# Performance work log

Hardware: AMD Instinct MI355X
Metric: run time of the kernel (lower is better)

## Reference

```python
import jax, jax.numpy as jnp
import numpy as np

# Module constants (from init_kwargs)
P = 0.1          # deletion probability (error_prob)
B, L, V = 4096, 128, 64   # batch, max_len, vocab_size


def setup_inputs() -> dict:
    key = jax.random.key(0)
    k1, k2, k3 = jax.random.split(key, 3)
    # messages/probs are relaxed one-hot distributions over the vocab
    messages = jax.nn.softmax(jax.random.normal(k1, (B, L, V), dtype=jnp.float32), axis=-1)
    probs = jax.nn.softmax(jax.random.normal(k2, (B, L, V), dtype=jnp.float32), axis=-1)
    # Bernoulli(P) deletion targets (module draws these from its own generator)
    target_mask = jax.random.uniform(k3, (B, L)) < P
    return {"messages": messages, "probs": probs, "target_mask": target_mask}


def _process_noise(messages, probs, target_mask):
    """Training-mode DeletionChannel.gs with apply_noise=True.

    The torch shift() loop (O(L) sequential masked rolls) is exactly stream
    compaction: kept symbols move to the front in order, and the last
    n_deleted positions are overwritten with the EOS one-hot [1,0,...,0].
    A single stable argsort on the deletion mask gives destination order.
    """
    _, Ln, Vn = messages.shape
    # stable sort keys: kept (0) before deleted (1), order preserved within each
    order = jnp.argsort(target_mask.astype(jnp.int32), axis=1, stable=True)  # [B,L]
    shifted = jnp.take_along_axis(messages, order[:, :, None], axis=1)        # [B,L,V]
    n_deleted = target_mask.sum(axis=1, keepdims=True)                        # [B,1]
    # positions j with (L-1-j) < n_deleted  <=>  j >= L - n_deleted
    eos_tail = jnp.arange(Ln)[None, :] >= (Ln - n_deleted)                    # [B,L]
    eos = jnp.zeros((Vn,), messages.dtype).at[0].set(1.0)
    out_messages = jnp.where(eos_tail[:, :, None], eos, shifted)
    # probs: non-EOS mass scaled by (1-p); EOS absorbs the remainder
    tail = probs[..., 1:] * (1.0 - P)
    out_probs = jnp.concatenate([1.0 - tail.sum(-1, keepdims=True), tail], axis=-1)
    return out_messages, out_probs


def reference(messages, probs, target_mask):
    # forward() returns (process(noise=True), process(noise=False));
    # the noise-free branch is the identity, so we return the noisy pair
    # stacked into one array: [2, B, L, V].
    out_m, out_p = _process_noise(messages, probs, target_mask)
    return jnp.stack([out_m, out_p])
```

## Files before the change

### kernel.cpp

```cpp
#include <hip/hip_runtime.h>

constexpr int Bn = 4096;
constexpr int Ln = 128;
constexpr int Vn = 64;
constexpr float KEEP = 0.9f;

__global__ __launch_bounds__(256) void deletion_channel_kernel(
    const float* __restrict__ msgs,
    const float* __restrict__ probs,
    const int* __restrict__ mask,
    float* __restrict__ out)
{
    const int b   = blockIdx.x;
    const int tid = threadIdx.x;
    const int lane = tid & 63;
    const int wave = tid >> 6;

    __shared__ int s_src[Ln];
    __shared__ int s_wavecnt[2];

    bool kept = false;
    int rank = 0;
    if (tid < Ln) kept = (mask[(size_t)b * Ln + tid] == 0);
    if (wave < 2) {
        unsigned long long bal = __ballot(kept);
        rank = __popcll(bal & ((1ull << lane) - 1ull));
        if (lane == 0) s_wavecnt[wave] = (int)__popcll(bal);
    }
    __syncthreads();
    if (tid < Ln && kept) {
        const int off = (wave == 1) ? s_wavecnt[0] : 0;
        s_src[off + rank] = tid;
    }
    __syncthreads();
    const int nkept = s_wavecnt[0] + s_wavecnt[1];

    const size_t rowbase = (size_t)b * (Ln * Vn);

    {
        const float4* __restrict__ src4 = (const float4*)(msgs + rowbase);
        float4* __restrict__ dst4       = (float4*)(out + rowbase);
        constexpr int TOT4 = Ln * Vn / 4;
        #pragma unroll
        for (int it = 0; it < TOT4 / 256; ++it) {
            const int idx = it * 256 + tid;
            const int j = idx >> 4;
            const int q = idx & 15;
            float4 v;
            if (j < nkept) {
                v = src4[(s_src[j] << 4) + q];
            } else {
                v = make_float4((q == 0) ? 1.0f : 0.0f, 0.0f, 0.0f, 0.0f);
            }
            dst4[idx] = v;
        }
    }

    {
        const float4* __restrict__ src4 = (const float4*)(probs + rowbase);
        float4* __restrict__ dst4 = (float4*)(out + (size_t)Bn * Ln * Vn + rowbase);
        constexpr int TOT4 = Ln * Vn / 4;
        #pragma unroll
        for (int it = 0; it < TOT4 / 256; ++it) {
            const int idx = it * 256 + tid;
            const int q = idx & 15;
            const float4 p = src4[idx];
            float s = p.x + p.y + p.z + p.w;
            if (q == 0) s -= p.x;
            s += __shfl_xor(s, 1);
            s += __shfl_xor(s, 2);
            s += __shfl_xor(s, 4);
            s += __shfl_xor(s, 8);
            float4 o = make_float4(p.x * KEEP, p.y * KEEP, p.z * KEEP, p.w * KEEP);
            if (q == 0) o.x = 1.0f - KEEP * s;
            dst4[idx] = o;
        }
    }
}

extern "C" void kernel_launch(void* const* d_in, const int* in_sizes, int n_in,
                              void* d_out, int out_size, void* d_ws, size_t ws_size,
                              hipStream_t stream) {
    const float* msgs  = (const float*)d_in[0];
    const float* probs = (const float*)d_in[1];
    const int*   mask  = (const int*)d_in[2];
    float* out = (float*)d_out;

    deletion_channel_kernel<<<Bn, 256, 0, stream>>>(msgs, probs, mask, out);
}
```

Before: 430.4 us.

## Split into separate msgs/probs kernels with nontemporal loads and stores

Splits the fused kernel into two launches: one compacts messages per batch row, the other processes probs over two rows per block. All global loads and stores become nontemporal builtins on ext_vector float4 types, so the streaming data bypasses cache retention. The probs kernel no longer waits on the mask prefix or the shared-memory syncs. In exchange it adds a second kernel launch and drops the overlap of the two streams within one block.

```diff
diff --git a/kernel.cpp b/kernel.cpp
--- a/kernel.cpp
+++ b/kernel.cpp
@@ -5,14 +5,15 @@
 constexpr int Vn = 64;
 constexpr float KEEP = 0.9f;
 
-__global__ __launch_bounds__(256) void deletion_channel_kernel(
+typedef float f32x4 __attribute__((ext_vector_type(4)));
+
+__global__ __launch_bounds__(256) void deletion_msgs_kernel(
     const float* __restrict__ msgs,
-    const float* __restrict__ probs,
     const int* __restrict__ mask,
     float* __restrict__ out)
 {
-    const int b   = blockIdx.x;
-    const int tid = threadIdx.x;
+    const int b    = blockIdx.x;
+    const int tid  = threadIdx.x;
     const int lane = tid & 63;
     const int wave = tid >> 6;
 
@@ -36,45 +37,47 @@
     const int nkept = s_wavecnt[0] + s_wavecnt[1];
 
     const size_t rowbase = (size_t)b * (Ln * Vn);
+    const f32x4* __restrict__ src4 = (const f32x4*)(msgs + rowbase);
+    f32x4* __restrict__ dst4       = (f32x4*)(out + rowbase);
+    constexpr int TOT4 = Ln * Vn / 4;
+    #pragma unroll
+    for (int it = 0; it < TOT4 / 256; ++it) {
+        const int idx = it * 256 + tid;
+        const int j = idx >> 4;
+        const int q = idx & 15;
+        f32x4 v;
+        if (j < nkept) {
+            v = __builtin_nontemporal_load(&src4[(s_src[j] << 4) + q]);
+        } else {
+            v = (f32x4){(q == 0) ? 1.0f : 0.0f, 0.0f, 0.0f, 0.0f};
+        }
+        __builtin_nontemporal_store(v, &dst4[idx]);
+    }
+}
 
-    {
-        const float4* __restrict__ src4 = (const float4*)(msgs + rowbase);
-        float4* __restrict__ dst4       = (float4*)(out + rowbase);
-        constexpr int TOT4 = Ln * Vn / 4;
-        #pragma unroll
-        for (int it = 0; it < TOT4 / 256; ++it) {
-            const int idx = it * 256 + tid;
-            const int j = idx >> 4;
-            const int q = idx & 15;
-            float4 v;
-            if (j < nkept) {
-                v = src4[(s_src[j] << 4) + q];
-            } else {
-                v = make_float4((q == 0) ? 1.0f : 0.0f, 0.0f, 0.0f, 0.0f);
-            }
-            dst4[idx] = v;
-        }
-    }
-
-    {
-        const float4* __restrict__ src4 = (const float4*)(probs + rowbase);
-        float4* __restrict__ dst4 = (float4*)(out + (size_t)Bn * Ln * Vn + rowbase);
-        constexpr int TOT4 = Ln * Vn / 4;
-        #pragma unroll
-        for (int it = 0; it < TOT4 / 256; ++it) {
-            const int idx = it * 256 + tid;
-            const int q = idx & 15;
-            const float4 p = src4[idx];
-            float s = p.x + p.y + p.z + p.w;
-            if (q == 0) s -= p.x;
-            s += __shfl_xor(s, 1);
-            s += __shfl_xor(s, 2);
-            s += __shfl_xor(s, 4);
-            s += __shfl_xor(s, 8);
-            float4 o = make_float4(p.x * KEEP, p.y * KEEP, p.z * KEEP, p.w * KEEP);
-            if (q == 0) o.x = 1.0f - KEEP * s;
-            dst4[idx] = o;
-        }
+__global__ __launch_bounds__(256) void deletion_probs_kernel(
+    const float* __restrict__ probs,
+    float* __restrict__ out)
+{
+    const int tid = threadIdx.x;
+    const size_t base = (size_t)blockIdx.x * (2 * Ln * Vn / 4);
+    const f32x4* __restrict__ src4 = (const f32x4*)probs + base;
+    f32x4* __restrict__ dst4 = (f32x4*)(out + (size_t)Bn * Ln * Vn) + base;
+    constexpr int TOT4 = 2 * Ln * Vn / 4;
+    #pragma unroll
+    for (int it = 0; it < TOT4 / 256; ++it) {
+        const int idx = it * 256 + tid;
+        const int q = idx & 15;
+        const f32x4 p = __builtin_nontemporal_load(&src4[idx]);
+        float s = p.x + p.y + p.z + p.w;
+        if (q == 0) s -= p.x;
+        s += __shfl_xor(s, 1);
+        s += __shfl_xor(s, 2);
+        s += __shfl_xor(s, 4);
+        s += __shfl_xor(s, 8);
+        f32x4 o = p * KEEP;
+        if (q == 0) o.x = 1.0f - KEEP * s;
+        __builtin_nontemporal_store(o, &dst4[idx]);
     }
 }
 
@@ -86,5 +89,6 @@
     const int*   mask  = (const int*)d_in[2];
     float* out = (float*)d_out;
 
-    deletion_channel_kernel<<<Bn, 256, 0, stream>>>(msgs, probs, mask, out);
+    deletion_msgs_kernel<<<Bn, 256, 0, stream>>>(msgs, mask, out);
+    deletion_probs_kernel<<<Bn / 2, 256, 0, stream>>>(probs, out);
 }
```

After: 420.9 us. 1.02x faster.
